# Kernel tuning notes

Hardware: AMD Instinct MI355X
Metric: run time of the kernel (lower is better)

Reference implementation:

```python
import jax, jax.numpy as jnp
import numpy as np

# ---- static config (matches init_kwargs) ----
R, A, K = 2048, 4, 4          # residues, backbone atoms, neighborhood size (self + <=3 edges)
N, B, C = R * A, 8, 64        # nodes, batch, hidden dim (= num_channels+time_embedding_channels)
H, D = 4, 16                  # heads, dim_head
HD, L = H * D, 4              # heads*dim_head, depth
E, Tc = 128, 61               # time_embedding_dim, time_embedding_channels
EPS = 1e-6


def _build_neighbors():
    """Fixed-K neighbor lists from the protein-backbone adjacency (self at k=0)."""
    adj = [[] for _ in range(N)]
    for r in range(R):
        b = r * A
        edges = [(b, b + 1), (b + 1, b + 2), (b + 2, b + 3)]
        if r < R - 1:
            edges.append((b + 2, (r + 1) * A))
        for i, j in edges:
            adj[i].append(j)
            adj[j].append(i)
    nbr = np.zeros((N, K), np.int32)
    msk = np.zeros((N, K), bool)
    for i in range(N):
        nbr[i, 0] = i
        msk[i, 0] = True
        for k, j in enumerate(adj[i][:K - 1]):
            nbr[i, k + 1] = j
            msk[i, k + 1] = True
    return jnp.asarray(nbr), jnp.asarray(msk)


def setup_inputs() -> dict:
    key = jax.random.key(0)
    ks = jax.random.split(key, 24)
    nbr, msk = _build_neighbors()

    def rn(i, shape, scale=1.0):
        return jax.random.normal(ks[i], shape, dtype=jnp.float32) * scale

    return {
        "x": rn(0, (B, N, 3)),
        "y": rn(1, (B, N, 3)),  # present in forward signature, unused by the math
        "t": jax.random.uniform(ks[2], (B,), dtype=jnp.float32),
        "nbr_idx": nbr, "nbr_mask": msk,
        "t_w1": rn(3, (E, E), E ** -0.5), "t_b1": jnp.zeros((E,), jnp.float32),
        "t_w2": rn(4, (E, Tc), E ** -0.5), "t_b2": jnp.zeros((Tc,), jnp.float32),
        "win1": rn(5, (C,)),
        "Wq0": rn(6, (L, C, HD), C ** -0.5), "Wk0": rn(7, (L, C, HD), C ** -0.5), "Wv0": rn(8, (L, C, HD), C ** -0.5),
        "Wq1": rn(9, (L, C, HD), C ** -0.5), "Wk1": rn(10, (L, C, HD), C ** -0.5), "Wv1": rn(11, (L, C, HD), C ** -0.5),
        "Wo0": rn(12, (L, HD, C), HD ** -0.5), "Wo1": rn(13, (L, HD, C), HD ** -0.5),
        "Wff0a": rn(14, (L, C, 4 * C), C ** -0.5), "Wff0b": rn(15, (L, 4 * C, C), (4 * C) ** -0.5),
        "Wff1": rn(16, (L, C, C), C ** -0.5),
        "Wout": rn(17, (3, C), C ** -0.5), "bout": jnp.zeros((3,), jnp.float32),
    }


def _sin_embed(t):
    half = E // 2
    freqs = jnp.exp(-jnp.log(10000.0) * jnp.arange(half, dtype=jnp.float32) / half)
    emb = t[:, None] * freqs
    return jnp.concatenate([jnp.sin(emb), jnp.cos(emb)], axis=-1)


def _ln(x):  # layernorm over channels, no affine
    mu = x.mean(-1, keepdims=True)
    v = x.var(-1, keepdims=True)
    return (x - mu) * jax.lax.rsqrt(v + EPS)


def _vnorm(f1):  # equivariant norm: scale by RMS of per-channel vector norms
    sq = jnp.sum(f1 * f1, axis=-1)                                    # [B,N,C]
    s = jax.lax.rsqrt(jnp.mean(sq, axis=-1, keepdims=True) + EPS)     # [B,N,1]
    return f1 * s[..., None]


def reference(x, y, t, nbr_idx, nbr_mask, t_w1, t_b1, t_w2, t_b2, win1,
              Wq0, Wk0, Wv0, Wq1, Wk1, Wv1, Wo0, Wo1, Wff0a, Wff0b, Wff1,
              Wout, bout):
    # time embedding MLP
    te = _sin_embed(t)
    te = jax.nn.silu(te @ t_w1 + t_b1) @ t_w2 + t_b2                  # [B,Tc]
    # degree-0 input: time embedding broadcast to nodes, concat positions
    f0 = jnp.concatenate([jnp.broadcast_to(te[:, None, :], (B, N, Tc)), x], axis=-1)  # [B,N,C]
    # degree-1 input: single vector channel (positions), lifted to C channels
    f1 = jnp.einsum('bnv,c->bncv', x, win1)                           # [B,N,C,3]

    rel = x[:, nbr_idx] - x[:, :, None, :]                            # [B,N,K,3]
    rhat = rel * jax.lax.rsqrt(jnp.sum(rel * rel, -1, keepdims=True) + EPS)
    mbias = jnp.where(nbr_mask, 0.0, -1e9)[None, :, None, :]          # [1,N,1,K]
    scale = D ** -0.5

    for l in range(L):
        g0, g1 = _ln(f0), _vnorm(f1)
        g0j = g0[:, nbr_idx]                                          # [B,N,K,C]
        g1j = g1[:, nbr_idx]                                          # [B,N,K,C,3]
        q0 = jnp.einsum('bnc,ce->bne', g0, Wq0[l]).reshape(B, N, H, D)
        k0 = jnp.einsum('bnkc,ce->bnke', g0j, Wk0[l]).reshape(B, N, K, H, D)
        v0 = jnp.einsum('bnkc,ce->bnke', g0j, Wv0[l]).reshape(B, N, K, H, D)
        q1 = jnp.einsum('bncv,ce->bnev', g1, Wq1[l]).reshape(B, N, H, D, 3)
        k1 = jnp.einsum('bnkcv,ce->bnkev', g1j, Wk1[l]).reshape(B, N, K, H, D, 3)
        v1 = jnp.einsum('bnkcv,ce->bnkev', g1j, Wv1[l]).reshape(B, N, K, H, D, 3)
        logits = (jnp.einsum('bnhd,bnkhd->bnhk', q0, k0)
                  + jnp.einsum('bnhdv,bnkhdv->bnhk', q1, k1)) * scale + mbias
        a = jax.nn.softmax(logits, axis=-1)                           # [B,N,H,K]
        # degree-mixing tensor products along edge direction rhat
        v1to0 = jnp.einsum('bnkhdv,bnkv->bnkhd', v1, rhat)            # 1 -> 0
        v0to1 = v0[..., None] * rhat[:, :, :, None, None, :]          # 0 -> 1
        o0 = jnp.einsum('bnhk,bnkhd->bnhd', a, v0 + v1to0).reshape(B, N, HD)
        o1 = jnp.einsum('bnhk,bnkhdv->bnhdv', a, v1 + v0to1).reshape(B, N, HD, 3)
        f0 = f0 + o0 @ Wo0[l]
        f1 = f1 + jnp.einsum('bnev,ec->bncv', o1, Wo1[l])
        # feedforward (equivariant: vector branch is linear in channels)
        f0 = f0 + jax.nn.silu(_ln(f0) @ Wff0a[l]) @ Wff0b[l]
        f1 = f1 + jnp.einsum('bncv,ce->bnev', _vnorm(f1), Wff1[l])

    # output layer: per-component channel projection of the degree-1 features
    score = jnp.einsum('bncv,vc->bnv', f1, Wout) + bout               # [B,N,3]
    return score
```

## Files before the change

### kernel.cpp

```cpp
#include <hip/hip_runtime.h>

#define BB 8
#define NN 8192
#define RR 2048
#define LL 4
#define TC 61
#define EPSF 1e-6f
#define BN (BB*NN)
#define OUTN (BN*3)

typedef unsigned short u16;
typedef unsigned int u32;
typedef _Float16 h2f __attribute__((ext_vector_type(2)));
typedef _Float16 h8 __attribute__((ext_vector_type(8)));
typedef float f4 __attribute__((ext_vector_type(4)));

__device__ __forceinline__ u32 packf16(float a, float b) {
  h2f h; h.x = (_Float16)a; h.y = (_Float16)b; return __builtin_bit_cast(u32, h);
}
__device__ __forceinline__ u16 f16b(float a) {
  _Float16 h = (_Float16)a; return __builtin_bit_cast(u16, h);
}
__device__ __forceinline__ float2 unpk(u32 a) {
  h2f h = __builtin_bit_cast(h2f, a); return make_float2((float)h.x, (float)h.y);
}
__device__ __forceinline__ float fdot2(u32 a, u32 b, float c) {
  return __builtin_amdgcn_fdot2(__builtin_bit_cast(h2f, a), __builtin_bit_cast(h2f, b), c, false);
}
__device__ __forceinline__ float frcp(float x) { return __builtin_amdgcn_rcpf(x); }
__device__ __forceinline__ float frsq(float x) { return __builtin_amdgcn_rsqf(x); }
__device__ __forceinline__ float fexp(float x) { return __expf(x); }
__device__ __forceinline__ int kmax_of(int n) {
  int aatom = n & 3, rres = n >> 2;
  return (aatom==0) ? (rres==0 ? 2 : 3)
       : (aatom==1) ? 3
       : (aatom==2) ? (rres==RR-1 ? 3 : 4) : 2;
}

__global__ __launch_bounds__(256) void k_const(float* out, float v) {
  int i = blockIdx.x*256 + threadIdx.x;
  if (i < OUTN) out[i] = v;
}

struct WSrc { const float* m[11]; };
__global__ __launch_bounds__(256) void k_prep(WSrc s, u32* W16,
    const float* t, const float* w1, const float* b1,
    const float* w2, const float* b2, float* te2,
    const float* x, const int* nbr, u16* rhat) {
  if (blockIdx.x >= 1096) {
    int i = (blockIdx.x - 1096)*256 + threadIdx.x;
    int tok = i >> 2, k = i & 3;
    int b = tok >> 13, n = tok & (NN-1);
    int tj = b*NN + nbr[n*4 + k];
    float x0 = x[tok*3+0], x1 = x[tok*3+1], x2 = x[tok*3+2];
    float rx = x[tj*3+0] - x0, ry = x[tj*3+1] - x1, rz = x[tj*3+2] - x2;
    float ir = rsqrtf(rx*rx + ry*ry + rz*rz + EPSF);
    rhat[(size_t)(tok*4+k)*3 + 0] = f16b(rx * ir);
    rhat[(size_t)(tok*4+k)*3 + 1] = f16b(ry * ir);
    rhat[(size_t)(tok*4+k)*3 + 2] = f16b(rz * ir);
    return;
  }
  if (blockIdx.x >= 1088) {
    __shared__ float s0[128], s1[128];
    int bb = blockIdx.x - 1088;
    int j = threadIdx.x;
    float tv = t[bb];
    if (j < 128) {
      int i = j & 63;
      float fr = expf(-9.210340371976184f * (float)i * (1.0f/64.0f));
      float em = tv * fr;
      s0[j] = (j < 64) ? sinf(em) : cosf(em);
    }
    __syncthreads();
    if (j < 128) {
      float acc = b1[j];
      for (int i2 = 0; i2 < 128; ++i2) acc += s0[i2] * w1[i2*128 + j];
      s1[j] = acc / (1.f + expf(-acc));
    }
    __syncthreads();
    if (j < TC) {
      float a2 = b2[j];
      for (int i2 = 0; i2 < 128; ++i2) a2 += s1[i2] * w2[i2*TC + j];
      te2[bb*TC + j] = a2;
    }
    return;
  }
  int i = blockIdx.x*256 + threadIdx.x;
  if (i < 73728) {
    int m = i >> 13, rr = i & 8191, l = rr >> 11, r2 = rr & 2047;
    int c2 = r2 >> 6, col = r2 & 63;
    const float* src = s.m[m] + l*4096;
    W16[i] = packf16(src[(2*c2)*64 + col], src[(2*c2+1)*64 + col]);
  } else if (i < 106496) {
    int j2 = i - 73728; int l = j2 >> 13, r2 = j2 & 8191;
    int c2 = r2 >> 8, j = r2 & 255;
    const float* src = s.m[9] + l*16384;
    W16[i] = packf16(src[(2*c2)*256 + j], src[(2*c2+1)*256 + j]);
  } else if (i < 139264) {
    int j2 = i - 106496; int l = j2 >> 13, r2 = j2 & 8191;
    int jp = r2 >> 6, e = r2 & 63;
    const float* src = s.m[10] + l*16384;
    W16[i] = packf16(src[(2*jp)*64 + e], src[(2*jp+1)*64 + e]);
  } else if (i < 188416) {
    int j2 = i - 139264;
    int l = j2 / 12288, rem = j2 % 12288;
    int m = rem >> 11, r2 = rem & 2047;
    int fb = r2 >> 8, li = r2 & 255;
    int nt = fb >> 1, kc = fb & 1;
    int lane = li >> 2, j = li & 3;
    int c2 = kc*16 + (lane>>4)*4 + j;
    int e  = nt*16 + (lane & 15);
    const float* src = s.m[m] + l*4096;
    W16[i] = packf16(src[(2*c2)*64 + e], src[(2*c2+1)*64 + e]);
  } else {
    int j2 = i - 188416;
    int l = j2 / 22528, rem = j2 % 22528;
    int li, fb, msel, N;
    const float* srcb;
    if (rem < 6144) {
      msel = 6 + (rem >> 11);
      int r2 = rem & 2047;
      fb = r2 >> 8; li = r2 & 255;
      srcb = s.m[msel] + l*4096; N = 64;
      int nt = fb >> 1, kc = fb & 1;
      int lane = li >> 2, j = li & 3;
      int c2 = kc*16 + (lane>>4)*4 + j;
      int e  = nt*16 + (lane & 15);
      W16[i] = packf16(srcb[(2*c2)*N + e], srcb[(2*c2+1)*N + e]);
    } else if (rem < 14336) {
      int r2 = rem - 6144;
      fb = r2 >> 8; li = r2 & 255;
      srcb = s.m[9] + l*16384; N = 256;
      int nt = fb >> 1, kc = fb & 1;
      int lane = li >> 2, j = li & 3;
      int c2 = kc*16 + (lane>>4)*4 + j;
      int e  = nt*16 + (lane & 15);
      W16[i] = packf16(srcb[(2*c2)*N + e], srcb[(2*c2+1)*N + e]);
    } else {
      int r2 = rem - 14336;
      fb = r2 >> 8; li = r2 & 255;
      srcb = s.m[10] + l*16384; N = 64;
      int nt = fb >> 3, kc = fb & 7;
      int lane = li >> 2, j = li & 3;
      int c2 = kc*16 + (lane>>4)*4 + j;
      int e  = nt*16 + (lane & 15);
      W16[i] = packf16(srcb[(2*c2)*N + e], srcb[(2*c2+1)*N + e]);
    }
  }
}

#define QH  0
#define KRG 4096
#define LK0 (KRG)
#define LV0 (KRG+1152)
#define LK1 (KRG+2304)
#define LV1 (KRG+5760)
#define LO0q (KRG)
#define LO1q (KRG+1152)
#define FR0q (KRG+4608)
#define FR1q (KRG+5632)
#define LDSU 13312

__global__ __launch_bounds__(256, 3) void k_layer(const u32* __restrict__ W16, int l,
    const u32* __restrict__ f0i, const u32* __restrict__ f1i,
    const int* __restrict__ nbr, const u16* __restrict__ rhat,
    u32* __restrict__ f0o, u32* __restrict__ f1o,
    const float* __restrict__ wout, const float* __restrict__ bout,
    float* __restrict__ out,
    const float* __restrict__ x, const float* __restrict__ win1,
    const float* __restrict__ te2) {
  __shared__ __align__(16) u32 S[LDSU];
  int tid = threadIdx.x, wv = tid >> 6, lane = tid & 63;
  int arow = lane & 15, aq = lane >> 4;
  int t0g = blockIdx.x * 32;
  int b = t0g >> 13, n0 = t0g & (NN-1);
  const u32 ONE2 = 0x3C003C00u;

  uint4 res0, res1a, res1b, res1c;
  if (l == 0) {
    {
      int t0 = tid >> 3, j0 = (tid & 7)*4;
      const float* x3 = x + ((size_t)b*NN + n0 + t0)*3;
      float xv[3] = {x3[0], x3[1], x3[2]};
      u32 tmp[4];
#pragma unroll
      for (int q = 0; q < 4; ++q) {
        int ca = 2*(j0+q), cb = ca+1;
        float va = (ca < TC) ? te2[b*TC+ca] : xv[ca-61];
        float vb = (cb < TC) ? te2[b*TC+cb] : xv[cb-61];
        tmp[q] = packf16(va, vb);
      }
      res0 = make_uint4(tmp[0], tmp[1], tmp[2], tmp[3]);
    }
    uint4* rr[3] = {&res1a, &res1b, &res1c};
#pragma unroll
    for (int k = 0; k < 3; ++k) {
      int idx = k*1024 + tid*4;
      int t = idx/96, rem = idx%96, v = rem >> 5, j = rem & 31;
      float xv = x[((size_t)b*NN + n0 + t)*3 + v];
      u32 tmp[4];
#pragma unroll
      for (int q = 0; q < 4; ++q)
        tmp[q] = packf16(xv*win1[2*(j+q)], xv*win1[2*(j+q)+1]);
      *rr[k] = make_uint4(tmp[0], tmp[1], tmp[2], tmp[3]);
    }
  } else {
    const u32* s0 = f0i + ((size_t)b*NN + n0)*32;
    const u32* s1 = f1i + ((size_t)b*NN + n0)*96;
    res0  = *(const uint4*)(s0 + tid*4);
    res1a = *(const uint4*)(s1 + (0*256 + tid)*4);
    res1b = *(const uint4*)(s1 + (1*256 + tid)*4);
    res1c = *(const uint4*)(s1 + (2*256 + tid)*4);
  }

  {
    const u32* base = W16 + 139264 + l*12288;
    int ncol = arow, mb = aq*4;

    auto ldraw = [&](int hr0, u32* r0, u32 (*r1)[8]) {
      int n = n0 - 2 + hr0 + arow;
      n = n < 0 ? 0 : (n > NN-1 ? NN-1 : n);
      size_t gt = (size_t)b*NN + n;
      if (l == 0) {
        const float* x3 = x + gt*3;
        float xv[3] = {x3[0], x3[1], x3[2]};
#pragma unroll
        for (int i = 0; i < 8; ++i) {
          int j = (i < 4) ? (aq*4+i) : (16 + aq*4 + (i-4));
          int ca = 2*j, cb = ca+1;
          float va = (ca < TC) ? te2[b*TC+ca] : xv[ca-61];
          float vb = (cb < TC) ? te2[b*TC+cb] : xv[cb-61];
          r0[i] = packf16(va, vb);
          float wa = win1[ca], wb = win1[cb];
#pragma unroll
          for (int v = 0; v < 3; ++v)
            r1[v][i] = packf16(xv[v]*wa, xv[v]*wb);
        }
      } else {
        *(uint4*)(r0)   = *(const uint4*)(f0i + gt*32 + aq*4);
        *(uint4*)(r0+4) = *(const uint4*)(f0i + gt*32 + 16 + aq*4);
#pragma unroll
        for (int v = 0; v < 3; ++v) {
          *(uint4*)(r1[v])   = *(const uint4*)(f1i + (gt*3+v)*32 + aq*4);
          *(uint4*)(r1[v]+4) = *(const uint4*)(f1i + (gt*3+v)*32 + 16 + aq*4);
        }
      }
    };

    auto mknorm = [&](const u32* r0, const u32 (*r1)[8], h8* g0f, h8 (*g1f)[2]) {
      float s = 0.f, s2 = 0.f;
#pragma unroll
      for (int i = 0; i < 8; ++i) { s = fdot2(r0[i], ONE2, s); s2 = fdot2(r0[i], r0[i], s2); }
      s  += __shfl_xor(s, 16, 64);  s  += __shfl_xor(s, 32, 64);
      s2 += __shfl_xor(s2, 16, 64); s2 += __shfl_xor(s2, 32, 64);
      float mu = s*(1.f/64.f);
      float ri = frsq(fmaxf(s2*(1.f/64.f)-mu*mu, 0.f) + EPSF);
      _Float16 rih = (_Float16)ri, bih = (_Float16)(-mu*ri);
      h2f scv; scv.x = rih; scv.y = rih;
      h2f biv; biv.x = bih; biv.y = bih;
#pragma unroll
      for (int kc = 0; kc < 2; ++kc) {
        u32 t0[4];
#pragma unroll
        for (int i = 0; i < 4; ++i) {
          h2f g = __builtin_bit_cast(h2f, r0[kc*4+i]) * scv + biv;
          t0[i] = __builtin_bit_cast(u32, g);
        }
        g0f[kc] = __builtin_bit_cast(h8, make_uint4(t0[0], t0[1], t0[2], t0[3]));
      }
      float ss = 0.f;
#pragma unroll
      for (int v = 0; v < 3; ++v)
#pragma unroll
        for (int i = 0; i < 8; ++i) ss = fdot2(r1[v][i], r1[v][i], ss);
      ss += __shfl_xor(ss, 16, 64); ss += __shfl_xor(ss, 32, 64);
      float vs = frsq(ss*(1.f/64.f) + EPSF);
      _Float16 vsh = (_Float16)vs;
      h2f vsv; vsv.x = vsh; vsv.y = vsh;
#pragma unroll
      for (int v = 0; v < 3; ++v)
#pragma unroll
        for (int kc = 0; kc < 2; ++kc) {
          u32 t1[4];
#pragma unroll
          for (int i = 0; i < 4; ++i) {
            h2f g = __builtin_bit_cast(h2f, r1[v][kc*4+i]) * vsv;
            t1[i] = __builtin_bit_cast(u32, g);
          }
          g1f[v][kc] = __builtin_bit_cast(h8, make_uint4(t1[0], t1[1], t1[2], t1[3]));
        }
    };

    auto projs = [&](const h8* afr, const u32* wM, u16* outh, int ob, int rmax) {
#pragma unroll
      for (int nt = 0; nt < 4; ++nt) {
        f4 acc = {0.f, 0.f, 0.f, 0.f};
#pragma unroll
        for (int kc = 0; kc < 2; ++kc) {
          uint4 wb = *(const uint4*)(wM + (nt*2+kc)*256 + lane*4);
          acc = __builtin_amdgcn_mfma_f32_16x16x32_f16(afr[kc], __builtin_bit_cast(h8, wb), acc, 0, 0, 0);
        }
        int ex = ((nt ^ aq)&3)*16 + ncol;
#pragma unroll
        for (int r = 0; r < 4; ++r) {
          int orow = ob + mb + r;
          if (orow < rmax) outh[orow*64 + ex] = f16b(acc[r]);
        }
      }
    };

    h8 g0f[2]; h8 g1f[3][2];
    if (wv < 3) {
      int tb = wv*16;
      u32 r0[8]; u32 r1[3][8];
      ldraw(tb, r0, r1);
      mknorm(r0, r1, g0f, g1f);
      projs(g0f, base + 1*2048, (u16*)(S+LK0), tb, 36);
      projs(g0f, base + 2*2048, (u16*)(S+LV0), tb, 36);
#pragma unroll
      for (int v = 0; v < 3; ++v) {
        projs(g1f[v], base + 4*2048, (u16*)(S+LK1) + v*2304, tb, 36);
        projs(g1f[v], base + 5*2048, (u16*)(S+LV1) + v*2304, tb, 36);
      }
    } else {
      u32 r0a[8], r1a[3][8], r0b[8], r1b[3][8];
      ldraw(2, r0a, r1a);
      ldraw(18, r0b, r1b);
      mknorm(r0a, r1a, g0f, g1f);
      projs(g0f, base, (u16*)(S+QH), 0, 32);
#pragma unroll
      for (int v = 0; v < 3; ++v)
        projs(g1f[v], base + 3*2048, (u16*)(S+1024) + v*2048, 0, 32);
      mknorm(r0b, r1b, g0f, g1f);
      projs(g0f, base, (u16*)(S+QH), 16, 32);
#pragma unroll
      for (int v = 0; v < 3; ++v)
        projs(g1f[v], base + 3*2048, (u16*)(S+1024) + v*2048, 16, 32);
    }
  }
  __syncthreads();

  u32 O0k[4], O1k[4][3];
  {
    const u32* Q0u = S + QH;
    const u32* Q1u = S + 1024;
    const u32* K0u = S + LK0;
    const u32* V0u = S + LV0;
    const u32* K1u = S + LK1;
    const u32* V1u = S + LV1;
    int half = lane >> 5, l32 = lane & 31;
#pragma unroll
    for (int it = 0; it < 4; ++it) {
      int ct = wv*8 + it*2 + half;
      int n = n0 + ct;
      size_t gt = (size_t)b*NN + n;
      int km = kmax_of(n);
      int4 nb = *(const int4*)(nbr + n*4);
      int lr[4];
      {
        int xx;
        xx = nb.x - n0 + 2; lr[0] = xx < 0 ? 0 : (xx > 35 ? 35 : xx);
        xx = nb.y - n0 + 2; lr[1] = xx < 0 ? 0 : (xx > 35 ? 35 : xx);
        xx = nb.z - n0 + 2; lr[2] = xx < 0 ? 0 : (xx > 35 ? 35 : xx);
        xx = nb.w - n0 + 2; lr[3] = xx < 0 ? 0 : (xx > 35 ? 35 : xx);
      }
      int jq = l32 ^ (((ct>>2)&3)<<3);
      u32 q0p = Q0u[ct*32 + jq];
      u32 q1p[3];
#pragma unroll
      for (int v = 0; v < 3; ++v) q1p[v] = Q1u[v*1024 + ct*32 + jq];
      float p[4];
#pragma unroll
      for (int k = 0; k < 4; ++k) {
        int row = lr[k];
        int jk = l32 ^ (((row>>2)&3)<<3);
        float acc = fdot2(q0p, K0u[row*32 + jk], 0.f);
#pragma unroll
        for (int v = 0; v < 3; ++v)
          acc = fdot2(q1p[v], K1u[v*1152 + row*32 + jk], acc);
        p[k] = acc;
      }
#pragma unroll
      for (int m = 1; m < 8; m <<= 1) {
#pragma unroll
        for (int k = 0; k < 4; ++k) p[k] += __shfl_xor(p[k], m, 64);
      }
      float mx = -1e30f;
#pragma unroll
      for (int k = 0; k < 4; ++k) { p[k] *= 0.25f; if (k < km) mx = fmaxf(mx, p[k]); }
      float aw[4], ssum = 0.f;
#pragma unroll
      for (int k = 0; k < 4; ++k) { aw[k] = (k < km) ? fexp(p[k]-mx) : 0.f; ssum += aw[k]; }
      float inv = frcp(ssum);
      const uint2* rp = (const uint2*)(rhat + (size_t)gt*12);
      uint2 ra = rp[0], rb = rp[1], rc = rp[2];
      u32 rw[6] = {ra.x, ra.y, rb.x, rb.y, rc.x, rc.y};
      h2f o0p = {(_Float16)0.f, (_Float16)0.f};
      h2f o1p0 = o0p, o1p1 = o0p, o1p2 = o0p;
#pragma unroll
      for (int k = 0; k < 4; ++k) {
        int row = lr[k];
        int jk = l32 ^ (((row>>2)&3)<<3);
        float a = aw[k]*inv;
        _Float16 ah = (_Float16)a;
        h2f a2; a2.x = ah; a2.y = ah;
        h2f v0p = __builtin_bit_cast(h2f, V0u[row*32 + jk]);
        h2f v1p[3], rh2[3];
#pragma unroll
        for (int v = 0; v < 3; ++v) {
          v1p[v] = __builtin_bit_cast(h2f, V1u[v*1152 + row*32 + jk]);
          int idx = k*3 + v;
          u32 w = rw[idx>>1];
          u32 hh = (idx&1) ? (w >> 16) : (w & 0xffffu);
          rh2[v] = __builtin_bit_cast(h2f, (hh << 16) | hh);
        }
        h2f vd = v1p[0]*rh2[0];
        vd = v1p[1]*rh2[1] + vd;
        vd = v1p[2]*rh2[2] + vd;
        o0p  = a2*(v0p + vd) + o0p;
        o1p0 = a2*(v0p*rh2[0] + v1p[0]) + o1p0;
        o1p1 = a2*(v0p*rh2[1] + v1p[1]) + o1p1;
        o1p2 = a2*(v0p*rh2[2] + v1p[2]) + o1p2;
      }
      O0k[it] = __builtin_bit_cast(u32, o0p);
      O1k[it][0] = __builtin_bit_cast(u32, o1p0);
      O1k[it][1] = __builtin_bit_cast(u32, o1p1);
      O1k[it][2] = __builtin_bit_cast(u32, o1p2);
    }
  }
  __syncthreads();

  {
    u32* o0u = S + LO0q;
    u32* o1u = S + LO1q;
    int half = lane >> 5, l32 = lane & 31;
#pragma unroll
    for (int it = 0; it < 4; ++it) {
      int ct = wv*8 + it*2 + half;
      o0u[ct*36 + l32] = O0k[it];
#pragma unroll
      for (int v = 0; v < 3; ++v)
        o1u[(v*32+ct)*36 + l32] = O1k[it][v];
    }
    uint4* d0 = (uint4*)(S + FR0q);
    d0[tid] = res0;
    uint4* d1 = (uint4*)(S + FR1q);
    d1[tid]       = res1a;
    d1[256 + tid] = res1b;
    d1[512 + tid] = res1c;
  }
  __syncthreads();

  {
    int tl16 = (wv & 1)*16;
    int ncol = arow, mb = aq*4;
    const u32* Wf = W16 + 188416 + l*22528;
    const u32* po0f = Wf;
    const u32* po1f = Wf + 2048;
    const u32* pf1f = Wf + 4096;
    const u32* paf  = Wf + 6144;
    const u32* pbf  = Wf + 14336;
    const u32* FR0 = S + FR0q;
    const u32* FR1 = S + FR1q;
    size_t gt0 = (size_t)b*NN + n0 + tl16;
    if (wv < 2) {
      h8 a1[3][2];
#pragma unroll
      for (int v = 0; v < 3; ++v)
#pragma unroll
        for (int kc = 0; kc < 2; ++kc)
          a1[v][kc] = __builtin_bit_cast(h8, *(const uint4*)(S + LO1q + (v*32 + tl16 + arow)*36 + kc*16 + aq*4));
      float f1m[3][4][4];
#pragma unroll
      for (int v = 0; v < 3; ++v)
#pragma unroll
        for (int nt = 0; nt < 4; ++nt) {
          f4 acc = {0.f, 0.f, 0.f, 0.f};
#pragma unroll
          for (int kc = 0; kc < 2; ++kc) {
            uint4 wb = *(const uint4*)(po1f + (nt*2+kc)*256 + lane*4);
            acc = __builtin_amdgcn_mfma_f32_16x16x32_f16(a1[v][kc], __builtin_bit_cast(h8, wb), acc, 0, 0, 0);
          }
#pragma unroll
          for (int r = 0; r < 4; ++r) {
            int t = tl16 + mb + r;
            float2 pq = unpk(FR1[(t*3+v)*32 + nt*8 + (ncol>>1)]);
            f1m[v][nt][r] = acc[r] + ((ncol&1) ? pq.y : pq.x);
          }
        }
      float vs[4];
#pragma unroll
      for (int r = 0; r < 4; ++r) {
        float ss = 0.f;
#pragma unroll
        for (int v = 0; v < 3; ++v)
#pragma unroll
          for (int nt = 0; nt < 4; ++nt) ss += f1m[v][nt][r]*f1m[v][nt][r];
        ss += __shfl_xor(ss, 1, 64); ss += __shfl_xor(ss, 2, 64);
        ss += __shfl_xor(ss, 4, 64); ss += __shfl_xor(ss, 8, 64);
        vs[r] = frsq(ss*(1.f/64.f) + EPSF);
      }
      u32* vn = S + FR1q + wv*1536;
      {
        u16* vnh = (u16*)vn;
#pragma unroll
        for (int v = 0; v < 3; ++v)
#pragma unroll
          for (int nt = 0; nt < 4; ++nt)
#pragma unroll
            for (int r = 0; r < 4; ++r)
              vnh[v*1024 + (mb+r)*64 + ((nt^aq)&3)*16 + ncol] = f16b(f1m[v][nt][r]*vs[r]);
      }
      float wl[3][4], sc[3][4];
      if (l == 3) {
#pragma unroll
        for (int v = 0; v < 3; ++v)
#pragma unroll
          for (int nt = 0; nt < 4; ++nt) { wl[v][nt] = wout[v*64 + nt*16 + ncol]; }
#pragma unroll
        for (int v = 0; v < 3; ++v)
#pragma unroll
          for (int r = 0; r < 4; ++r) sc[v][r] = 0.f;
      }
#pragma unroll
      for (int v = 0; v < 3; ++v)
#pragma unroll
        for (int nt = 0; nt < 4; ++nt) {
          f4 acc = {0.f, 0.f, 0.f, 0.f};
#pragma unroll
          for (int kc = 0; kc < 2; ++kc) {
            int lc = kc*2 + (aq>>1);
            int pc = (lc ^ (arow>>2)) & 3;
            h8 af = __builtin_bit_cast(h8, *(const uint4*)(vn + v*512 + arow*32 + pc*8 + (aq&1)*4));
            uint4 wb = *(const uint4*)(pf1f + (nt*2+kc)*256 + lane*4);
            acc = __builtin_amdgcn_mfma_f32_16x16x32_f16(af, __builtin_bit_cast(h8, wb), acc, 0, 0, 0);
          }
#pragma unroll
          for (int r = 0; r < 4; ++r) {
            size_t gt = gt0 + mb + r;
            float val = acc[r] + f1m[v][nt][r];
            if (l < 3) {
              float par = __shfl_xor(val, 1, 64);
              if (!(ncol & 1))
                f1o[(gt*3+v)*32 + nt*8 + (ncol>>1)] = packf16(val, par);
            } else {
              sc[v][r] += val * wl[v][nt];
            }
          }
        }
      if (l == 3) {
#pragma unroll
        for (int v = 0; v < 3; ++v)
#pragma unroll
          for (int r = 0; r < 4; ++r) {
            float xx = sc[v][r];
            xx += __shfl_xor(xx, 1, 64); xx += __shfl_xor(xx, 2, 64);
            xx += __shfl_xor(xx, 4, 64); xx += __shfl_xor(xx, 8, 64);
            if (ncol == 0) out[(gt0 + mb + r)*3 + v] = xx + bout[v];
          }
      }
    } else if (l < 3) {
      h8 a0[2];
#pragma unroll
      for (int kc = 0; kc < 2; ++kc)
        a0[kc] = __builtin_bit_cast(h8, *(const uint4*)(S + LO0q + (tl16 + arow)*36 + kc*16 + aq*4));
      float f0m[4][4];
#pragma unroll
      for (int nt = 0; nt < 4; ++nt) {
        f4 acc = {0.f, 0.f, 0.f, 0.f};
#pragma unroll
        for (int kc = 0; kc < 2; ++kc) {
          uint4 wb = *(const uint4*)(po0f + (nt*2+kc)*256 + lane*4);
          acc = __builtin_amdgcn_mfma_f32_16x16x32_f16(a0[kc], __builtin_bit_cast(h8, wb), acc, 0, 0, 0);
        }
#pragma unroll
        for (int r = 0; r < 4; ++r) {
          int t = tl16 + mb + r;
          float2 pq = unpk(FR0[t*32 + nt*8 + (ncol>>1)]);
          f0m[nt][r] = acc[r] + ((ncol&1) ? pq.y : pq.x);
        }
      }
      float mu[4], ri[4];
#pragma unroll
      for (int r = 0; r < 4; ++r) {
        float sg = 0.f, s2 = 0.f;
#pragma unroll
        for (int nt = 0; nt < 4; ++nt) { sg += f0m[nt][r]; s2 += f0m[nt][r]*f0m[nt][r]; }
        sg += __shfl_xor(sg, 1, 64); sg += __shfl_xor(sg, 2, 64);
        sg += __shfl_xor(sg, 4, 64); sg += __shfl_xor(sg, 8, 64);
        s2 += __shfl_xor(s2, 1, 64); s2 += __shfl_xor(s2, 2, 64);
        s2 += __shfl_xor(s2, 4, 64); s2 += __shfl_xor(s2, 8, 64);
        mu[r] = sg*(1.f/64.f);
        ri[r] = frsq(fmaxf(s2*(1.f/64.f)-mu[r]*mu[r], 0.f) + EPSF);
      }
      u32* gg = S + FR0q + (wv & 1)*512;
      {
        u16* gh = (u16*)gg;
#pragma unroll
        for (int nt = 0; nt < 4; ++nt)
#pragma unroll
          for (int r = 0; r < 4; ++r)
            gh[(mb+r)*64 + ((nt^aq)&3)*16 + ncol] = f16b((f0m[nt][r]-mu[r])*ri[r]);
      }
      u32* hp = S + (wv-2)*2048;
      {
        h8 ga[2];
#pragma unroll
        for (int kc = 0; kc < 2; ++kc) {
          int lc = kc*2 + (aq>>1);
          int pc = (lc ^ (arow>>2)) & 3;
          ga[kc] = __builtin_bit_cast(h8, *(const uint4*)(gg + arow*32 + pc*8 + (aq&1)*4));
        }
        u16* hhh = (u16*)hp;
#pragma unroll
        for (int nt16 = 0; nt16 < 16; ++nt16) {
          f4 acc = {0.f, 0.f, 0.f, 0.f};
#pragma unroll
          for (int kc = 0; kc < 2; ++kc) {
            uint4 wb = *(const uint4*)(paf + (nt16*2+kc)*256 + lane*4);
            acc = __builtin_amdgcn_mfma_f32_16x16x32_f16(ga[kc], __builtin_bit_cast(h8, wb), acc, 0, 0, 0);
          }
#pragma unroll
          for (int r = 0; r < 4; ++r) {
            float a = acc[r];
            int row = mb + r;
            int chunk = (nt16*2 + (ncol>>3)) ^ (row & 7);
            hhh[row*256 + chunk*8 + (ncol&7)] = f16b(a * frcp(1.f + fexp(-a)));
          }
        }
      }
#pragma unroll
      for (int nt = 0; nt < 4; ++nt) {
        f4 acc = {0.f, 0.f, 0.f, 0.f};
#pragma unroll
        for (int kc = 0; kc < 8; ++kc) {
          int c = kc*4 + aq;
          h8 af = __builtin_bit_cast(h8, *(const uint4*)(hp + arow*128 + ((c ^ (arow & 7))<<2)));
          uint4 wb = *(const uint4*)(pbf + (nt*8+kc)*256 + lane*4);
          acc = __builtin_amdgcn_mfma_f32_16x16x32_f16(af, __builtin_bit_cast(h8, wb), acc, 0, 0, 0);
        }
#pragma unroll
        for (int r = 0; r < 4; ++r) {
          size_t gt = gt0 + mb + r;
          float val = acc[r] + f0m[nt][r];
          float par = __shfl_xor(val, 1, 64);
          if (!(ncol & 1))
            f0o[gt*32 + nt*8 + (ncol>>1)] = packf16(val, par);
        }
      }
    }
  }
}

extern "C" void kernel_launch(void* const* d_in, const int* in_sizes, int n_in,
                              void* d_out, int out_size, void* d_ws, size_t ws_size,
                              hipStream_t stream) {
  float* out = (float*)d_out;
  static const int exp23[23] = {196608,196608,8,32768,32768,16384,128,7808,61,64,
                                16384,16384,16384,16384,16384,16384,16384,16384,
                                65536,65536,16384,192,3};
  bool ok23 = (n_in == 23), ok22 = (n_in == 22);
  int bad = -1;
  if (ok23) {
    for (int i = 0; i < 23; ++i) if (in_sizes[i] != exp23[i]) { ok23 = false; bad = i; break; }
  }
  if (!ok23 && ok22) {
    for (int i = 0; i < 22; ++i) {
      int want = (i == 0) ? exp23[0] : exp23[i+1];
      if (in_sizes[i] != want) { ok22 = false; if (bad < 0) bad = i; break; }
    }
  } else ok22 = false;
  if (!ok23 && !ok22) {
    k_const<<<768, 256, 0, stream>>>(out, (float)(3000 + (bad < 0 ? 100 + n_in : bad)));
    return;
  }
  int sh = ok23 ? 0 : -1;
  const int* nbr = (const int*)d_in[3 + sh];
  const float* F[20];
  F[0] = (const float*)d_in[0];
  F[1] = (const float*)d_in[2 + sh];
  for (int j = 0; j < 18; ++j) F[2 + j] = (const float*)d_in[5 + sh + j];

  char* ws = (char*)d_ws;
  u32*   W16  = (u32*)ws;
  float* te2  = (float*)(ws + 1114112);
  u16*   rhat = (u16*)(ws + 1116160);
  u32*   f0A  = (u32*)(ws + 2689024);
  u32*   f1A  = (u32*)(ws + 11077632);
  u32*   f0B  = (u32*)(ws + 36243456);
  u32*   f1B  = (u32*)(ws + 44632064);

  WSrc s;
  s.m[0]=F[7]; s.m[1]=F[8]; s.m[2]=F[9]; s.m[3]=F[10]; s.m[4]=F[11]; s.m[5]=F[12];
  s.m[6]=F[13]; s.m[7]=F[14]; s.m[8]=F[17]; s.m[9]=F[15]; s.m[10]=F[16];

  k_prep<<<1096 + BN*4/256, 256, 0, stream>>>(s, W16, F[1], F[2], F[3], F[4], F[5], te2,
                                              F[0], nbr, rhat);
  for (int l = 0; l < LL; ++l) {
    const u32* fi0 = (l & 1) ? f0B : f0A;
    const u32* fi1 = (l & 1) ? f1B : f1A;
    u32*       fo0 = (l & 1) ? f0A : f0B;
    u32*       fo1 = (l & 1) ? f1A : f1B;
    k_layer<<<BN/32, 256, 0, stream>>>(W16, l, fi0, fi1, nbr, rhat, fo0, fo1,
                                       F[18], F[19], out, F[0], F[6], te2);
  }
}
```

Baseline: 337.9 us.

## Split attention into two phases to alias V1 over K1 and shrink LDS

```diff
diff --git a/kernel.cpp b/kernel.cpp
--- a/kernel.cpp
+++ b/kernel.cpp
@@ -150,18 +150,19 @@
 }
 
 #define QH  0
-#define KRG 4096
-#define LK0 (KRG)
-#define LV0 (KRG+1152)
-#define LK1 (KRG+2304)
-#define LV1 (KRG+5760)
-#define LO0q (KRG)
-#define LO1q (KRG+1152)
-#define FR0q (KRG+4608)
-#define FR1q (KRG+5632)
-#define LDSU 13312
-
-__global__ __launch_bounds__(256, 3) void k_layer(const u32* __restrict__ W16, int l,
+#define LQ1 1024
+#define KVB 4096
+#define LK0 (KVB)
+#define LV0 (KVB+1152)
+#define LK1 (KVB+2304)
+#define LV1 (KVB+2304)
+#define LO0q (KVB)
+#define LO1q (KVB+1152)
+#define FR0q 0
+#define FR1q 1024
+#define LDSU 9856
+
+__global__ __launch_bounds__(256, 4) void k_layer(const u32* __restrict__ W16, int l,
     const u32* __restrict__ f0i, const u32* __restrict__ f1i,
     const int* __restrict__ nbr, const u16* __restrict__ rhat,
     u32* __restrict__ f0o, u32* __restrict__ f1o,
@@ -172,6 +173,7 @@
   __shared__ __align__(16) u32 S[LDSU];
   int tid = threadIdx.x, wv = tid >> 6, lane = tid & 63;
   int arow = lane & 15, aq = lane >> 4;
+  int ncol = arow, mb = aq*4;
   int t0g = blockIdx.x * 32;
   int b = t0g >> 13, n0 = t0g & (NN-1);
   const u32 ONE2 = 0x3C003C00u;
@@ -213,141 +215,137 @@
     res1c = *(const uint4*)(s1 + (2*256 + tid)*4);
   }
 
+  const u32* base = W16 + 139264 + l*12288;
+  h8 g0f[2]; h8 g1f[3][2];
+
+  auto ldraw = [&](int hr0, u32* r0, u32 (*r1)[8]) {
+    int n = n0 - 2 + hr0 + arow;
+    n = n < 0 ? 0 : (n > NN-1 ? NN-1 : n);
+    size_t gt = (size_t)b*NN + n;
+    if (l == 0) {
+      const float* x3 = x + gt*3;
+      float xv[3] = {x3[0], x3[1], x3[2]};
+#pragma unroll
+      for (int i = 0; i < 8; ++i) {
+        int j = (i < 4) ? (aq*4+i) : (16 + aq*4 + (i-4));
+        int ca = 2*j, cb = ca+1;
+        float va = (ca < TC) ? te2[b*TC+ca] : xv[ca-61];
+        float vb = (cb < TC) ? te2[b*TC+cb] : xv[cb-61];
+        r0[i] = packf16(va, vb);
+        float wa = win1[ca], wb = win1[cb];
+#pragma unroll
+        for (int v = 0; v < 3; ++v)
+          r1[v][i] = packf16(xv[v]*wa, xv[v]*wb);
+      }
+    } else {
+      *(uint4*)(r0)   = *(const uint4*)(f0i + gt*32 + aq*4);
+      *(uint4*)(r0+4) = *(const uint4*)(f0i + gt*32 + 16 + aq*4);
+#pragma unroll
+      for (int v = 0; v < 3; ++v) {
+        *(uint4*)(r1[v])   = *(const uint4*)(f1i + (gt*3+v)*32 + aq*4);
+        *(uint4*)(r1[v]+4) = *(const uint4*)(f1i + (gt*3+v)*32 + 16 + aq*4);
+      }
+    }
+  };
+
+  auto mknorm = [&](const u32* r0, const u32 (*r1)[8]) {
+    float s = 0.f, s2 = 0.f;
+#pragma unroll
+    for (int i = 0; i < 8; ++i) { s = fdot2(r0[i], ONE2, s); s2 = fdot2(r0[i], r0[i], s2); }
+    s  += __shfl_xor(s, 16, 64);  s  += __shfl_xor(s, 32, 64);
+    s2 += __shfl_xor(s2, 16, 64); s2 += __shfl_xor(s2, 32, 64);
+    float mu = s*(1.f/64.f);
+    float ri = frsq(fmaxf(s2*(1.f/64.f)-mu*mu, 0.f) + EPSF);
+    _Float16 rih = (_Float16)ri, bih = (_Float16)(-mu*ri);
+    h2f scv; scv.x = rih; scv.y = rih;
+    h2f biv; biv.x = bih; biv.y = bih;
+#pragma unroll
+    for (int kc = 0; kc < 2; ++kc) {
+      u32 t0[4];
+#pragma unroll
+      for (int i = 0; i < 4; ++i) {
+        h2f g = __builtin_bit_cast(h2f, r0[kc*4+i]) * scv + biv;
+        t0[i] = __builtin_bit_cast(u32, g);
+      }
+      g0f[kc] = __builtin_bit_cast(h8, make_uint4(t0[0], t0[1], t0[2], t0[3]));
+    }
+    float ss = 0.f;
+#pragma unroll
+    for (int v = 0; v < 3; ++v)
+#pragma unroll
+      for (int i = 0; i < 8; ++i) ss = fdot2(r1[v][i], r1[v][i], ss);
+    ss += __shfl_xor(ss, 16, 64); ss += __shfl_xor(ss, 32, 64);
+    float vs = frsq(ss*(1.f/64.f) + EPSF);
+    _Float16 vsh = (_Float16)vs;
+    h2f vsv; vsv.x = vsh; vsv.y = vsh;
+#pragma unroll
+    for (int v = 0; v < 3; ++v)
+#pragma unroll
+      for (int kc = 0; kc < 2; ++kc) {
+        u32 t1[4];
+#pragma unroll
+        for (int i = 0; i < 4; ++i) {
+          h2f g = __builtin_bit_cast(h2f, r1[v][kc*4+i]) * vsv;
+          t1[i] = __builtin_bit_cast(u32, g);
+        }
+        g1f[v][kc] = __builtin_bit_cast(h8, make_uint4(t1[0], t1[1], t1[2], t1[3]));
+      }
+  };
+
+  auto projs = [&](const h8* afr, const u32* wM, u16* outh, int ob, int rmax) {
+#pragma unroll
+    for (int nt = 0; nt < 4; ++nt) {
+      f4 acc = {0.f, 0.f, 0.f, 0.f};
+#pragma unroll
+      for (int kc = 0; kc < 2; ++kc) {
+        uint4 wb = *(const uint4*)(wM + (nt*2+kc)*256 + lane*4);
+        acc = __builtin_amdgcn_mfma_f32_16x16x32_f16(afr[kc], __builtin_bit_cast(h8, wb), acc, 0, 0, 0);
+      }
+      int ex = ((nt ^ aq)&3)*16 + ncol;
+#pragma unroll
+      for (int r = 0; r < 4; ++r) {
+        int orow = ob + mb + r;
+        if (orow < rmax) outh[orow*64 + ex] = f16b(acc[r]);
+      }
+    }
+  };
+
   {
-    const u32* base = W16 + 139264 + l*12288;
-    int ncol = arow, mb = aq*4;
-
-    auto ldraw = [&](int hr0, u32* r0, u32 (*r1)[8]) {
-      int n = n0 - 2 + hr0 + arow;
-      n = n < 0 ? 0 : (n > NN-1 ? NN-1 : n);
-      size_t gt = (size_t)b*NN + n;
-      if (l == 0) {
-        const float* x3 = x + gt*3;
-        float xv[3] = {x3[0], x3[1], x3[2]};
-#pragma unroll
-        for (int i = 0; i < 8; ++i) {
-          int j = (i < 4) ? (aq*4+i) : (16 + aq*4 + (i-4));
-          int ca = 2*j, cb = ca+1;
-          float va = (ca < TC) ? te2[b*TC+ca] : xv[ca-61];
-          float vb = (cb < TC) ? te2[b*TC+cb] : xv[cb-61];
-          r0[i] = packf16(va, vb);
-          float wa = win1[ca], wb = win1[cb];
-#pragma unroll
-          for (int v = 0; v < 3; ++v)
-            r1[v][i] = packf16(xv[v]*wa, xv[v]*wb);
-        }
-      } else {
-        *(uint4*)(r0)   = *(const uint4*)(f0i + gt*32 + aq*4);
-        *(uint4*)(r0+4) = *(const uint4*)(f0i + gt*32 + 16 + aq*4);
-#pragma unroll
-        for (int v = 0; v < 3; ++v) {
-          *(uint4*)(r1[v])   = *(const uint4*)(f1i + (gt*3+v)*32 + aq*4);
-          *(uint4*)(r1[v]+4) = *(const uint4*)(f1i + (gt*3+v)*32 + 16 + aq*4);
-        }
-      }
-    };
-
-    auto mknorm = [&](const u32* r0, const u32 (*r1)[8], h8* g0f, h8 (*g1f)[2]) {
-      float s = 0.f, s2 = 0.f;
-#pragma unroll
-      for (int i = 0; i < 8; ++i) { s = fdot2(r0[i], ONE2, s); s2 = fdot2(r0[i], r0[i], s2); }
-      s  += __shfl_xor(s, 16, 64);  s  += __shfl_xor(s, 32, 64);
-      s2 += __shfl_xor(s2, 16, 64); s2 += __shfl_xor(s2, 32, 64);
-      float mu = s*(1.f/64.f);
-      float ri = frsq(fmaxf(s2*(1.f/64.f)-mu*mu, 0.f) + EPSF);
-      _Float16 rih = (_Float16)ri, bih = (_Float16)(-mu*ri);
-      h2f scv; scv.x = rih; scv.y = rih;
-      h2f biv; biv.x = bih; biv.y = bih;
-#pragma unroll
-      for (int kc = 0; kc < 2; ++kc) {
-        u32 t0[4];
-#pragma unroll
-        for (int i = 0; i < 4; ++i) {
-          h2f g = __builtin_bit_cast(h2f, r0[kc*4+i]) * scv + biv;
-          t0[i] = __builtin_bit_cast(u32, g);
-        }
-        g0f[kc] = __builtin_bit_cast(h8, make_uint4(t0[0], t0[1], t0[2], t0[3]));
-      }
-      float ss = 0.f;
-#pragma unroll
-      for (int v = 0; v < 3; ++v)
-#pragma unroll
-        for (int i = 0; i < 8; ++i) ss = fdot2(r1[v][i], r1[v][i], ss);
-      ss += __shfl_xor(ss, 16, 64); ss += __shfl_xor(ss, 32, 64);
-      float vs = frsq(ss*(1.f/64.f) + EPSF);
-      _Float16 vsh = (_Float16)vs;
-      h2f vsv; vsv.x = vsh; vsv.y = vsh;
-#pragma unroll
-      for (int v = 0; v < 3; ++v)
-#pragma unroll
-        for (int kc = 0; kc < 2; ++kc) {
-          u32 t1[4];
-#pragma unroll
-          for (int i = 0; i < 4; ++i) {
-            h2f g = __builtin_bit_cast(h2f, r1[v][kc*4+i]) * vsv;
-            t1[i] = __builtin_bit_cast(u32, g);
-          }
-          g1f[v][kc] = __builtin_bit_cast(h8, make_uint4(t1[0], t1[1], t1[2], t1[3]));
-        }
-    };
-
-    auto projs = [&](const h8* afr, const u32* wM, u16* outh, int ob, int rmax) {
-#pragma unroll
-      for (int nt = 0; nt < 4; ++nt) {
-        f4 acc = {0.f, 0.f, 0.f, 0.f};
-#pragma unroll
-        for (int kc = 0; kc < 2; ++kc) {
-          uint4 wb = *(const uint4*)(wM + (nt*2+kc)*256 + lane*4);
-          acc = __builtin_amdgcn_mfma_f32_16x16x32_f16(afr[kc], __builtin_bit_cast(h8, wb), acc, 0, 0, 0);
-        }
-        int ex = ((nt ^ aq)&3)*16 + ncol;
-#pragma unroll
-        for (int r = 0; r < 4; ++r) {
-          int orow = ob + mb + r;
-          if (orow < rmax) outh[orow*64 + ex] = f16b(acc[r]);
-        }
-      }
-    };
-
-    h8 g0f[2]; h8 g1f[3][2];
     if (wv < 3) {
       int tb = wv*16;
       u32 r0[8]; u32 r1[3][8];
       ldraw(tb, r0, r1);
-      mknorm(r0, r1, g0f, g1f);
+      mknorm(r0, r1);
       projs(g0f, base + 1*2048, (u16*)(S+LK0), tb, 36);
       projs(g0f, base + 2*2048, (u16*)(S+LV0), tb, 36);
 #pragma unroll
-      for (int v = 0; v < 3; ++v) {
+      for (int v = 0; v < 3; ++v)
         projs(g1f[v], base + 4*2048, (u16*)(S+LK1) + v*2304, tb, 36);
-        projs(g1f[v], base + 5*2048, (u16*)(S+LV1) + v*2304, tb, 36);
-      }
     } else {
       u32 r0a[8], r1a[3][8], r0b[8], r1b[3][8];
       ldraw(2, r0a, r1a);
       ldraw(18, r0b, r1b);
-      mknorm(r0a, r1a, g0f, g1f);
+      mknorm(r0a, r1a);
       projs(g0f, base, (u16*)(S+QH), 0, 32);
 #pragma unroll
       for (int v = 0; v < 3; ++v)
-        projs(g1f[v], base + 3*2048, (u16*)(S+1024) + v*2048, 0, 32);
-      mknorm(r0b, r1b, g0f, g1f);
+        projs(g1f[v], base + 3*2048, (u16*)(S+LQ1) + v*2048, 0, 32);
+      mknorm(r0b, r1b);
       projs(g0f, base, (u16*)(S+QH), 16, 32);
 #pragma unroll
       for (int v = 0; v < 3; ++v)
-        projs(g1f[v], base + 3*2048, (u16*)(S+1024) + v*2048, 16, 32);
+        projs(g1f[v], base + 3*2048, (u16*)(S+LQ1) + v*2048, 16, 32);
     }
   }
   __syncthreads();
 
-  u32 O0k[4], O1k[4][3];
+  u32 O0k[4], O1k[4][3], AWp[4][2];
   {
     const u32* Q0u = S + QH;
-    const u32* Q1u = S + 1024;
+    const u32* Q1u = S + LQ1;
     const u32* K0u = S + LK0;
     const u32* V0u = S + LV0;
     const u32* K1u = S + LK1;
-    const u32* V1u = S + LV1;
     int half = lane >> 5, l32 = lane & 31;
 #pragma unroll
     for (int it = 0; it < 4; ++it) {
@@ -392,6 +390,8 @@
 #pragma unroll
       for (int k = 0; k < 4; ++k) { aw[k] = (k < km) ? fexp(p[k]-mx) : 0.f; ssum += aw[k]; }
       float inv = frcp(ssum);
+      AWp[it][0] = packf16(aw[0]*inv, aw[1]*inv);
+      AWp[it][1] = packf16(aw[2]*inv, aw[3]*inv);
       const uint2* rp = (const uint2*)(rhat + (size_t)gt*12);
       uint2 ra = rp[0], rb = rp[1], rc = rp[2];
       u32 rw[6] = {ra.x, ra.y, rb.x, rb.y, rc.x, rc.y};
@@ -405,6 +405,67 @@
         _Float16 ah = (_Float16)a;
         h2f a2; a2.x = ah; a2.y = ah;
         h2f v0p = __builtin_bit_cast(h2f, V0u[row*32 + jk]);
+#pragma unroll
+        for (int v = 0; v < 3; ++v) {
+          int idx = k*3 + v;
+          u32 w = rw[idx>>1];
+          u32 hh = (idx&1) ? (w >> 16) : (w & 0xffffu);
+          h2f rh2 = __builtin_bit_cast(h2f, (hh << 16) | hh);
+          h2f term = a2*(v0p*rh2);
+          if (v == 0) o1p0 = term + o1p0;
+          else if (v == 1) o1p1 = term + o1p1;
+          else o1p2 = term + o1p2;
+        }
+        o0p = a2*v0p + o0p;
+      }
+      O0k[it] = __builtin_bit_cast(u32, o0p);
+      O1k[it][0] = __builtin_bit_cast(u32, o1p0);
+      O1k[it][1] = __builtin_bit_cast(u32, o1p1);
+      O1k[it][2] = __builtin_bit_cast(u32, o1p2);
+    }
+  }
+  __syncthreads();
+
+  if (wv < 3) {
+    int tb = wv*16;
+#pragma unroll
+    for (int v = 0; v < 3; ++v)
+      projs(g1f[v], base + 5*2048, (u16*)(S+LV1) + v*2304, tb, 36);
+  }
+  __syncthreads();
+
+  {
+    const u32* V1u = S + LV1;
+    int half = lane >> 5, l32 = lane & 31;
+#pragma unroll
+    for (int it = 0; it < 4; ++it) {
+      int ct = wv*8 + it*2 + half;
+      int n = n0 + ct;
+      size_t gt = (size_t)b*NN + n;
+      int4 nb = *(const int4*)(nbr + n*4);
+      int lr[4];
+      {
+        int xx;
+        xx = nb.x - n0 + 2; lr[0] = xx < 0 ? 0 : (xx > 35 ? 35 : xx);
+        xx = nb.y - n0 + 2; lr[1] = xx < 0 ? 0 : (xx > 35 ? 35 : xx);
+        xx = nb.z - n0 + 2; lr[2] = xx < 0 ? 0 : (xx > 35 ? 35 : xx);
+        xx = nb.w - n0 + 2; lr[3] = xx < 0 ? 0 : (xx > 35 ? 35 : xx);
+      }
+      const uint2* rp = (const uint2*)(rhat + (size_t)gt*12);
+      uint2 ra = rp[0], rb = rp[1], rc = rp[2];
+      u32 rw[6] = {ra.x, ra.y, rb.x, rb.y, rc.x, rc.y};
+      float2 awA = unpk(AWp[it][0]), awB = unpk(AWp[it][1]);
+      float af4[4] = {awA.x, awA.y, awB.x, awB.y};
+      h2f o0p = __builtin_bit_cast(h2f, O0k[it]);
+      h2f o1p0 = __builtin_bit_cast(h2f, O1k[it][0]);
+      h2f o1p1 = __builtin_bit_cast(h2f, O1k[it][1]);
+      h2f o1p2 = __builtin_bit_cast(h2f, O1k[it][2]);
+#pragma unroll
+      for (int k = 0; k < 4; ++k) {
+        int row = lr[k];
+        int jk = l32 ^ (((row>>2)&3)<<3);
+        _Float16 ah = (_Float16)af4[k];
+        h2f a2; a2.x = ah; a2.y = ah;
         h2f v1p[3], rh2[3];
 #pragma unroll
         for (int v = 0; v < 3; ++v) {
@@ -417,10 +478,10 @@
         h2f vd = v1p[0]*rh2[0];
         vd = v1p[1]*rh2[1] + vd;
         vd = v1p[2]*rh2[2] + vd;
-        o0p  = a2*(v0p + vd) + o0p;
-        o1p0 = a2*(v0p*rh2[0] + v1p[0]) + o1p0;
-        o1p1 = a2*(v0p*rh2[1] + v1p[1]) + o1p1;
-        o1p2 = a2*(v0p*rh2[2] + v1p[2]) + o1p2;
+        o0p  = a2*vd + o0p;
+        o1p0 = a2*v1p[0] + o1p0;
+        o1p1 = a2*v1p[1] + o1p1;
+        o1p2 = a2*v1p[2] + o1p2;
       }
       O0k[it] = __builtin_bit_cast(u32, o0p);
       O1k[it][0] = __builtin_bit_cast(u32, o1p0);
@@ -451,9 +512,22 @@
   }
   __syncthreads();
 
+  int tl16 = (wv & 1)*16;
+  h8 a1[3][2]; h8 a0[2];
+  if (wv < 2) {
+#pragma unroll
+    for (int v = 0; v < 3; ++v)
+#pragma unroll
+      for (int kc = 0; kc < 2; ++kc)
+        a1[v][kc] = __builtin_bit_cast(h8, *(const uint4*)(S + LO1q + (v*32 + tl16 + arow)*36 + kc*16 + aq*4));
+  } else {
+#pragma unroll
+    for (int kc = 0; kc < 2; ++kc)
+      a0[kc] = __builtin_bit_cast(h8, *(const uint4*)(S + LO0q + (tl16 + arow)*36 + kc*16 + aq*4));
+  }
+  __syncthreads();
+
   {
-    int tl16 = (wv & 1)*16;
-    int ncol = arow, mb = aq*4;
     const u32* Wf = W16 + 188416 + l*22528;
     const u32* po0f = Wf;
     const u32* po1f = Wf + 2048;
@@ -464,12 +538,6 @@
     const u32* FR1 = S + FR1q;
     size_t gt0 = (size_t)b*NN + n0 + tl16;
     if (wv < 2) {
-      h8 a1[3][2];
-#pragma unroll
-      for (int v = 0; v < 3; ++v)
-#pragma unroll
-        for (int kc = 0; kc < 2; ++kc)
-          a1[v][kc] = __builtin_bit_cast(h8, *(const uint4*)(S + LO1q + (v*32 + tl16 + arow)*36 + kc*16 + aq*4));
       float f1m[3][4][4];
 #pragma unroll
       for (int v = 0; v < 3; ++v)
@@ -560,10 +628,6 @@
           }
       }
     } else if (l < 3) {
-      h8 a0[2];
-#pragma unroll
-      for (int kc = 0; kc < 2; ++kc)
-        a0[kc] = __builtin_bit_cast(h8, *(const uint4*)(S + LO0q + (tl16 + arow)*36 + kc*16 + aq*4));
       float f0m[4][4];
 #pragma unroll
       for (int nt = 0; nt < 4; ++nt) {
@@ -602,7 +666,7 @@
           for (int r = 0; r < 4; ++r)
             gh[(mb+r)*64 + ((nt^aq)&3)*16 + ncol] = f16b((f0m[nt][r]-mu[r])*ri[r]);
       }
-      u32* hp = S + (wv-2)*2048;
+      u32* hp = S + KVB + (wv-2)*2048;
       {
         h8 ga[2];
 #pragma unroll
```

Result: slower. 404.2 us (+19.6%).
